# Optimization experiments

Measured on AMD Instinct MI355X. Metric: run time of the kernel, lower is better.

Reference implementation:

```python
import jax, jax.numpy as jnp
import numpy as np

VOCAB = 50000
DIM = 20      # vector_dim; must equal RNN hidden size per the classifier shape constraint
HID = 20
NCLS = 5
B, S = 16384, 256

def setup_inputs() -> dict:
    key = jax.random.key(0)
    k1, k2, k3, k4, k5, k6 = jax.random.split(key, 6)
    x = jax.random.randint(k1, (B, S), 0, VOCAB, dtype=jnp.int64)
    emb = jax.random.normal(k2, (VOCAB, DIM), dtype=jnp.float32)
    W_ih = jax.random.normal(k3, (HID, DIM), dtype=jnp.float32) * 0.1
    W_hh = jax.random.normal(k4, (HID, HID), dtype=jnp.float32) * 0.1
    W_cls = jax.random.normal(k5, (NCLS, DIM), dtype=jnp.float32) * 0.1
    b_cls = jax.random.normal(k6, (NCLS,), dtype=jnp.float32) * 0.1
    return {"x": x, "emb": emb, "W_ih": W_ih, "W_hh": W_hh, "W_cls": W_cls, "b_cls": b_cls}

def reference(x, emb, W_ih, W_hh, W_cls, b_cls):
    # padding_idx=0: row 0 of embedding is zero
    emb = emb.at[0].set(0.0)
    xe = emb[x]                                   # [B, S, DIM]
    # precompute input projection for all timesteps in one big matmul
    xp = jnp.einsum('bsd,hd->sbh', xe, W_ih)      # [S, B, HID]
    h0 = jnp.zeros((x.shape[0], HID), dtype=xe.dtype)

    def step(h, xt):
        h = jnp.tanh(xt + h @ W_hh.T)
        return h, None

    h_last, _ = jax.lax.scan(step, h0, xp)        # [B, HID]
    y_pred = h_last @ W_cls.T + b_cls             # [B, 5]
    return y_pred
```

## Files before the change

kernel.cpp:

```cpp
#include <hip/hip_runtime.h>
#include <hip/hip_bf16.h>

#define SEQ  256
#define DIM  20
#define NCLS 5
#define ALPHA 2.8853900817779268f

typedef short  bf16x8 __attribute__((ext_vector_type(8)));
typedef float  f32x4  __attribute__((ext_vector_type(4)));
typedef float  v2f    __attribute__((ext_vector_type(2)));

__device__ __forceinline__ v2f fast_tanh2_s(v2f xs) {
    v2f e;
    e.x = __builtin_amdgcn_exp2f(xs.x);
    e.y = __builtin_amdgcn_exp2f(xs.y);
    v2f d = e + 1.0f;
    const float r = __builtin_amdgcn_rcpf(d.x * d.y);
    v2f inv;
    inv.x = d.y * r;
    inv.y = d.x * r;
    return __builtin_elementwise_fma((v2f)(-2.0f), inv, (v2f)(1.0f));
}

__device__ __forceinline__ int cvt_pk_bf16(float lo, float hi) {
    int r;
    asm("v_cvt_pk_bf16_f32 %0, %1, %2" : "=v"(r) : "v"(lo), "v"(hi));
    return r;
}

__device__ __forceinline__ void pl32swap(int &a, int &b) {
    asm("v_permlane32_swap_b32 %0, %1" : "+v"(a), "+v"(b));
}

__device__ __forceinline__ int permk(int k) {
    return (k >= 4 && k < 8) ? k + 4 : (k >= 8 && k < 12) ? k - 4 : k;
}

union I4B { int i[4]; bf16x8 f; };

#define STEP(TIDX)                                                            \
    {                                                                          \
        const f32x4 loN = *(const f32x4*)(emb + (size_t)tokG0 * DIM + eoff0);  \
        const f32x4 hiN = *(const f32x4*)(emb + (size_t)tokG0 * DIM + eoff1);  \
        const bool  nzN = (tokG0 != 0);                                        \
        const int tokNew = xp[(TIDX)];                                         \
        const f32x4 acc1 = __builtin_amdgcn_mfma_f32_16x16x32_bf16(A1h, Bh.f, aePre1, 0, 0, 0); \
        const f32x4 acc0 = __builtin_amdgcn_mfma_f32_16x16x32_bf16(A0h, Bh.f, aePre0, 0, 0, 0); \
        I4B Be;                                                                \
        Be.i[0] = nzA ? cvt_pk_bf16(loA[0], loA[1]) : 0;                       \
        Be.i[1] = nzA ? cvt_pk_bf16(loA[2], loA[3]) : 0;                       \
        Be.i[2] = nzA ? cvt_pk_bf16(hiA[0], hiA[1]) : 0;                       \
        Be.i[3] = nzA ? cvt_pk_bf16(hiA[2], hiA[3]) : 0;                       \
        aePre0 = __builtin_amdgcn_mfma_f32_16x16x32_bf16(A0e, Be.f, zf, 0, 0, 0); \
        aePre1 = __builtin_amdgcn_mfma_f32_16x16x32_bf16(A1e, Be.f, zf, 0, 0, 0); \
        const v2f p2 = fast_tanh2_s((v2f){acc1[0], acc1[1]});                  \
        const v2f p3 = fast_tanh2_s((v2f){acc1[2], acc1[3]});                  \
        int tp0 = cvt_pk_bf16(p2.x, p2.y);                                     \
        int tp1 = cvt_pk_bf16(p3.x, p3.y);                                     \
        const v2f p0 = fast_tanh2_s((v2f){acc0[0], acc0[1]});                  \
        const v2f p1 = fast_tanh2_s((v2f){acc0[2], acc0[3]});                  \
        int w0 = cvt_pk_bf16(p0.x, p0.y);                                      \
        int w1 = cvt_pk_bf16(p1.x, p1.y);                                      \
        pl32swap(w0, tp0);                 \
        pl32swap(w1, tp1);                                                     \
        Bh.i[0] = w0; Bh.i[1] = w1; Bh.i[2] = tp0; Bh.i[3] = tp1;              \
        loA = loB; hiA = hiB; nzA = nzB;                                       \
        loB = loC; hiB = hiC; nzB = nzC;                                       \
        loC = loD; hiC = hiD; nzC = nzD;                                       \
        loD = loN; hiD = hiN; nzD = nzN;                                       \
        tokG0 = tokG1; tokG1 = tokG2; tokG2 = tokG3; tokG3 = tokNew;           \
    }

__global__ __launch_bounds__(256)
__attribute__((amdgpu_waves_per_eu(1, 1)))
void rnn_mfma(const int* __restrict__ x,
              const float* __restrict__ emb,
              const float* __restrict__ W_ih,
              const float* __restrict__ W_hh,
              const float* __restrict__ W_cls,
              const float* __restrict__ b_cls,
              float* __restrict__ out, int B)
{
    const int gtid = blockIdx.x * blockDim.x + threadIdx.x;
    const int wave = gtid >> 6;
    const int lane = (int)(threadIdx.x & 63);
    const int c = lane & 15;
    const int q = lane >> 4;
    const int row0 = wave * 16;
    if (row0 >= B) return;

    auto loadA = [&](const float* M, int U0, int ROWS, bool pk, float scale) {
        bf16x8 f;
        const int uu = U0 + c;
        const int ur = uu < ROWS ? uu : 0;
#pragma unroll
        for (int j = 0; j < 8; ++j) {
            const int kk = 8 * q + j;
            const int kp = pk ? permk(kk) : kk;
            const int kr = kp < DIM ? kp : 0;
            float v = M[ur * DIM + kr] * scale;
            v = (uu < ROWS && kk < DIM) ? v : 0.0f;
            __hip_bfloat16 hb = __float2bfloat16(v);
            f[j] = *reinterpret_cast<short*>(&hb);
        }
        return f;
    };
    const bf16x8 A0h = loadA(W_hh,  0, DIM,  true,  ALPHA);
    const bf16x8 A0e = loadA(W_ih,  0, DIM,  false, ALPHA);
    const bf16x8 A1h = loadA(W_hh, 16, DIM,  true,  ALPHA);
    const bf16x8 A1e = loadA(W_ih, 16, DIM,  false, ALPHA);
    const bf16x8 Acl = loadA(W_cls, 0, NCLS, true,  1.0f);

    float bias[4];
#pragma unroll
    for (int j = 0; j < 4; ++j) {
        const int idx = 4 * q + j;
        bias[j] = (idx < NCLS) ? b_cls[idx] : 0.0f;
    }

    const int eoff0 = (q == 0) ? 0 : (q == 1) ? 8 : 16;
    const int eoff1 = (q == 0) ? 4 : (q == 1) ? 12 : 16;

    const int* xp = x + (size_t)(row0 + c) * SEQ;
    const f32x4 zf = {0.0f, 0.0f, 0.0f, 0.0f};

    I4B Bh; Bh.i[0] = Bh.i[1] = Bh.i[2] = Bh.i[3] = 0;
    const int tk0 = xp[0];
    const int tk1 = xp[1];
    const int tk2 = xp[2];
    const int tk3 = xp[3];
    const int tk4 = xp[4];
    f32x4 aePre0, aePre1;
    {
        const f32x4 lo = *(const f32x4*)(emb + (size_t)tk0 * DIM + eoff0);
        const f32x4 hi = *(const f32x4*)(emb + (size_t)tk0 * DIM + eoff1);
        const bool nz = (tk0 != 0);
        I4B Be;
        Be.i[0] = nz ? cvt_pk_bf16(lo[0], lo[1]) : 0;
        Be.i[1] = nz ? cvt_pk_bf16(lo[2], lo[3]) : 0;
        Be.i[2] = nz ? cvt_pk_bf16(hi[0], hi[1]) : 0;
        Be.i[3] = nz ? cvt_pk_bf16(hi[2], hi[3]) : 0;
        aePre0 = __builtin_amdgcn_mfma_f32_16x16x32_bf16(A0e, Be.f, zf, 0, 0, 0);
        aePre1 = __builtin_amdgcn_mfma_f32_16x16x32_bf16(A1e, Be.f, zf, 0, 0, 0);
    }

    f32x4 loA, hiA, loB, hiB, loC, hiC, loD, hiD;
    bool nzA, nzB, nzC, nzD;
    loA = *(const f32x4*)(emb + (size_t)tk1 * DIM + eoff0);
    hiA = *(const f32x4*)(emb + (size_t)tk1 * DIM + eoff1);
    nzA = (tk1 != 0);
    loB = *(const f32x4*)(emb + (size_t)tk2 * DIM + eoff0);
    hiB = *(const f32x4*)(emb + (size_t)tk2 * DIM + eoff1);
    nzB = (tk2 != 0);
    loC = *(const f32x4*)(emb + (size_t)tk3 * DIM + eoff0);
    hiC = *(const f32x4*)(emb + (size_t)tk3 * DIM + eoff1);
    nzC = (tk3 != 0);
    loD = *(const f32x4*)(emb + (size_t)tk4 * DIM + eoff0);
    hiD = *(const f32x4*)(emb + (size_t)tk4 * DIM + eoff1);
    nzD = (tk4 != 0);
    int tokG0 = xp[5];
    int tokG1 = xp[6];
    int tokG2 = xp[7];
    int tokG3 = xp[8];

#pragma unroll 8
    for (int s = 0; s < 240; ++s) {
        STEP(s + 9)
    }
#pragma unroll 4
    for (int s = 240; s < SEQ; ++s) {
        STEP((s + 9 < SEQ) ? (s + 9) : (SEQ - 1))
    }

    const f32x4 y = __builtin_amdgcn_mfma_f32_16x16x32_bf16(Acl, Bh.f, zf, 0, 0, 0);
    float* orow = out + (size_t)(row0 + c) * NCLS;
    if (q == 0) {
        orow[0] = y[0] + bias[0];
        orow[1] = y[1] + bias[1];
        orow[2] = y[2] + bias[2];
        orow[3] = y[3] + bias[3];
    } else if (q == 1) {
        orow[4] = y[0] + bias[0];
    }
}

extern "C" void kernel_launch(void* const* d_in, const int* in_sizes, int n_in,
                              void* d_out, int out_size, void* d_ws, size_t ws_size,
                              hipStream_t stream) {
    const int*   x     = (const int*)d_in[0];
    const float* emb   = (const float*)d_in[1];
    const float* W_ih  = (const float*)d_in[2];
    const float* W_hh  = (const float*)d_in[3];
    const float* W_cls = (const float*)d_in[4];
    const float* b_cls = (const float*)d_in[5];
    float* out = (float*)d_out;

    const int B = in_sizes[0] / SEQ;
    const int threads = B * 4;
    const int block = 256;
    const int grid = (threads + block - 1) / block;
    rnn_mfma<<<grid, block, 0, stream>>>(x, emb, W_ih, W_hh, W_cls, b_cls, out, B);
}
```

Before: 68.56 us.

## Interleave two independent 16-row RNN tiles per wave to hide MFMA latency

Each wave now processes two independent 16-row batch tiles (P and Q) and interleaves their gather, MFMA, tanh and rotate phases so one tile's work fills the other's recurrence dependency stalls. The launch changes from 256-thread blocks with one tile per wave to 64-thread blocks with two tiles per wave, which halves the wave count. This costs roughly double the register state per wave, fewer resident waves overall, and assumes B is a multiple of 32.

```diff
diff --git a/kernel.cpp b/kernel.cpp
--- a/kernel.cpp
+++ b/kernel.cpp
@@ -38,56 +38,113 @@
 
 union I4B { int i[4]; bf16x8 f; };
 
-#define STEP(TIDX)                                                            \
-    {                                                                          \
-        const f32x4 loN = *(const f32x4*)(emb + (size_t)tokG0 * DIM + eoff0);  \
-        const f32x4 hiN = *(const f32x4*)(emb + (size_t)tokG0 * DIM + eoff1);  \
-        const bool  nzN = (tokG0 != 0);                                        \
-        const int tokNew = xp[(TIDX)];                                         \
-        const f32x4 acc1 = __builtin_amdgcn_mfma_f32_16x16x32_bf16(A1h, Bh.f, aePre1, 0, 0, 0); \
-        const f32x4 acc0 = __builtin_amdgcn_mfma_f32_16x16x32_bf16(A0h, Bh.f, aePre0, 0, 0, 0); \
+#define TILE_PROLOG(S, XP)                                                     \
+    I4B Bh##S; Bh##S.i[0] = Bh##S.i[1] = Bh##S.i[2] = Bh##S.i[3] = 0;          \
+    f32x4 aePre0##S, aePre1##S;                                                \
+    {                                                                          \
+        const int tk0 = (XP)[0];                                               \
+        const f32x4 lo = *(const f32x4*)(emb + (size_t)tk0 * DIM + eoff0);     \
+        const f32x4 hi = *(const f32x4*)(emb + (size_t)tk0 * DIM + eoff1);     \
+        const bool nz = (tk0 != 0);                       \
         I4B Be;                                                                \
-        Be.i[0] = nzA ? cvt_pk_bf16(loA[0], loA[1]) : 0;                       \
-        Be.i[1] = nzA ? cvt_pk_bf16(loA[2], loA[3]) : 0;                       \
-        Be.i[2] = nzA ? cvt_pk_bf16(hiA[0], hiA[1]) : 0;                       \
-        Be.i[3] = nzA ? cvt_pk_bf16(hiA[2], hiA[3]) : 0;                       \
-        aePre0 = __builtin_amdgcn_mfma_f32_16x16x32_bf16(A0e, Be.f, zf, 0, 0, 0); \
-        aePre1 = __builtin_amdgcn_mfma_f32_16x16x32_bf16(A1e, Be.f, zf, 0, 0, 0); \
-        const v2f p2 = fast_tanh2_s((v2f){acc1[0], acc1[1]});                  \
-        const v2f p3 = fast_tanh2_s((v2f){acc1[2], acc1[3]});                  \
+        Be.i[0] = nz ? cvt_pk_bf16(lo[0], lo[1]) : 0;                          \
+        Be.i[1] = nz ? cvt_pk_bf16(lo[2], lo[3]) : 0;                          \
+        Be.i[2] = nz ? cvt_pk_bf16(hi[0], hi[1]) : 0;                          \
+        Be.i[3] = nz ? cvt_pk_bf16(hi[2], hi[3]) : 0;                          \
+        aePre0##S = __builtin_amdgcn_mfma_f32_16x16x32_bf16(A0e, Be.f, zf, 0, 0, 0); \
+        aePre1##S = __builtin_amdgcn_mfma_f32_16x16x32_bf16(A1e, Be.f, zf, 0, 0, 0); \
+    }                                                                          \
+    const int tk1##S = (XP)[1], tk2##S = (XP)[2], tk3##S = (XP)[3], tk4##S = (XP)[4]; \
+    f32x4 loA##S, hiA##S, loB##S, hiB##S, loC##S, hiC##S, loD##S, hiD##S;      \
+    bool nzA##S, nzB##S, nzC##S, nzD##S;                                       \
+    loA##S = *(const f32x4*)(emb + (size_t)tk1##S * DIM + eoff0);              \
+    hiA##S = *(const f32x4*)(emb + (size_t)tk1##S * DIM + eoff1);              \
+    nzA##S = (tk1##S != 0);                                                    \
+    loB##S = *(const f32x4*)(emb + (size_t)tk2##S * DIM + eoff0);              \
+    hiB##S = *(const f32x4*)(emb + (size_t)tk2##S * DIM + eoff1);              \
+    nzB##S = (tk2##S != 0);                                                    \
+    loC##S = *(const f32x4*)(emb + (size_t)tk3##S * DIM + eoff0);              \
+    hiC##S = *(const f32x4*)(emb + (size_t)tk3##S * DIM + eoff1);              \
+    nzC##S = (tk3##S != 0);                                                    \
+    loD##S = *(const f32x4*)(emb + (size_t)tk4##S * DIM + eoff0);              \
+    hiD##S = *(const f32x4*)(emb + (size_t)tk4##S * DIM + eoff1);              \
+    nzD##S = (tk4##S != 0);                                                    \
+    int tokG0##S = (XP)[5], tokG1##S = (XP)[6], tokG2##S = (XP)[7], tokG3##S = (XP)[8];
+
+#define PH_GATHER(S, TIDX)                                                     \
+    const f32x4 loN##S = *(const f32x4*)(emb + (size_t)tokG0##S * DIM + eoff0);\
+    const f32x4 hiN##S = *(const f32x4*)(emb + (size_t)tokG0##S * DIM + eoff1);\
+    const bool  nzN##S = (tokG0##S != 0);                                      \
+    const int tokNew##S = xp##S[(TIDX)];
+
+#define PH_HMFMA(S)                                                            \
+    const f32x4 acc1##S = __builtin_amdgcn_mfma_f32_16x16x32_bf16(A1h, Bh##S.f, aePre1##S, 0, 0, 0); \
+    const f32x4 acc0##S = __builtin_amdgcn_mfma_f32_16x16x32_bf16(A0h, Bh##S.f, aePre0##S, 0, 0, 0);
+
+#define PH_EPATH(S)                                                            \
+    {                                                                          \
+        I4B Be;                                                                \
+        Be.i[0] = nzA##S ? cvt_pk_bf16(loA##S[0], loA##S[1]) : 0;              \
+        Be.i[1] = nzA##S ? cvt_pk_bf16(loA##S[2], loA##S[3]) : 0;              \
+        Be.i[2] = nzA##S ? cvt_pk_bf16(hiA##S[0], hiA##S[1]) : 0;              \
+        Be.i[3] = nzA##S ? cvt_pk_bf16(hiA##S[2], hiA##S[3]) : 0;              \
+        aePre0##S = __builtin_amdgcn_mfma_f32_16x16x32_bf16(A0e, Be.f, zf, 0, 0, 0); \
+        aePre1##S = __builtin_amdgcn_mfma_f32_16x16x32_bf16(A1e, Be.f, zf, 0, 0, 0); \
+    }
+
+#define PH_TANH(S)                                                             \
+    {                                                                          \
+        const v2f p2 = fast_tanh2_s((v2f){acc1##S[0], acc1##S[1]});            \
+        const v2f p3 = fast_tanh2_s((v2f){acc1##S[2], acc1##S[3]});            \
         int tp0 = cvt_pk_bf16(p2.x, p2.y);                                     \
         int tp1 = cvt_pk_bf16(p3.x, p3.y);                                     \
-        const v2f p0 = fast_tanh2_s((v2f){acc0[0], acc0[1]});                  \
-        const v2f p1 = fast_tanh2_s((v2f){acc0[2], acc0[3]});                  \
+        const v2f p0 = fast_tanh2_s((v2f){acc0##S[0], acc0##S[1]});            \
+        const v2f p1 = fast_tanh2_s((v2f){acc0##S[2], acc0##S[3]});            \
         int w0 = cvt_pk_bf16(p0.x, p0.y);                                      \
         int w1 = cvt_pk_bf16(p1.x, p1.y);                                      \
         pl32swap(w0, tp0);                 \
         pl32swap(w1, tp1);                                                     \
-        Bh.i[0] = w0; Bh.i[1] = w1; Bh.i[2] = tp0; Bh.i[3] = tp1;              \
-        loA = loB; hiA = hiB; nzA = nzB;                                       \
-        loB = loC; hiB = hiC; nzB = nzC;                                       \
-        loC = loD; hiC = hiD; nzC = nzD;                                       \
-        loD = loN; hiD = hiN; nzD = nzN;                                       \
-        tokG0 = tokG1; tokG1 = tokG2; tokG2 = tokG3; tokG3 = tokNew;           \
-    }
-
-__global__ __launch_bounds__(256)
+        Bh##S.i[0] = w0; Bh##S.i[1] = w1; Bh##S.i[2] = tp0; Bh##S.i[3] = tp1;  \
+    }
+
+#define PH_ROT(S)                                                              \
+    loA##S = loB##S; hiA##S = hiB##S; nzA##S = nzB##S;                         \
+    loB##S = loC##S; hiB##S = hiC##S; nzB##S = nzC##S;                         \
+    loC##S = loD##S; hiC##S = hiD##S; nzC##S = nzD##S;                         \
+    loD##S = loN##S; hiD##S = hiN##S; nzD##S = nzN##S;                         \
+    tokG0##S = tokG1##S; tokG1##S = tokG2##S; tokG2##S = tokG3##S; tokG3##S = tokNew##S;
+
+#define STEP2(TIDX)                                                            \
+    {                                                                          \
+        PH_GATHER(P, TIDX)                                                     \
+        PH_GATHER(Q, TIDX)                                                     \
+        PH_HMFMA(P)                                                            \
+        PH_HMFMA(Q)                                                            \
+        PH_EPATH(P)                                                            \
+        PH_EPATH(Q)                                                            \
+        PH_TANH(P)                                                             \
+        PH_TANH(Q)                                                             \
+        PH_ROT(P)                                                              \
+        PH_ROT(Q)                                                              \
+    }
+
+__global__ __launch_bounds__(64)
 __attribute__((amdgpu_waves_per_eu(1, 1)))
-void rnn_mfma(const int* __restrict__ x,
-              const float* __restrict__ emb,
-              const float* __restrict__ W_ih,
-              const float* __restrict__ W_hh,
-              const float* __restrict__ W_cls,
-              const float* __restrict__ b_cls,
-              float* __restrict__ out, int B)
+void rnn_mfma2(const int* __restrict__ x,
+               const float* __restrict__ emb,
+               const float* __restrict__ W_ih,
+               const float* __restrict__ W_hh,
+               const float* __restrict__ W_cls,
+               const float* __restrict__ b_cls,
+               float* __restrict__ out, int B)
 {
-    const int gtid = blockIdx.x * blockDim.x + threadIdx.x;
-    const int wave = gtid >> 6;
+    const int wave = (int)blockIdx.x;
     const int lane = (int)(threadIdx.x & 63);
     const int c = lane & 15;
     const int q = lane >> 4;
-    const int row0 = wave * 16;
-    if (row0 >= B) return;
+    const int row0P = wave * 32;
+    const int row0Q = row0P + 16;
+    if (row0P >= B) return;
 
     auto loadA = [&](const float* M, int U0, int ROWS, bool pk, float scale) {
         bf16x8 f;
@@ -121,66 +178,45 @@
     const int eoff0 = (q == 0) ? 0 : (q == 1) ? 8 : 16;
     const int eoff1 = (q == 0) ? 4 : (q == 1) ? 12 : 16;
 
-    const int* xp = x + (size_t)(row0 + c) * SEQ;
+    const int* xpP = x + (size_t)(row0P + c) * SEQ;
+    const int* xpQ = x + (size_t)(row0Q + c) * SEQ;
     const f32x4 zf = {0.0f, 0.0f, 0.0f, 0.0f};
 
-    I4B Bh; Bh.i[0] = Bh.i[1] = Bh.i[2] = Bh.i[3] = 0;
-    const int tk0 = xp[0];
-    const int tk1 = xp[1];
-    const int tk2 = xp[2];
-    const int tk3 = xp[3];
-    const int tk4 = xp[4];
-    f32x4 aePre0, aePre1;
-    {
-        const f32x4 lo = *(const f32x4*)(emb + (size_t)tk0 * DIM + eoff0);
-        const f32x4 hi = *(const f32x4*)(emb + (size_t)tk0 * DIM + eoff1);
-        const bool nz = (tk0 != 0);
-        I4B Be;
-        Be.i[0] = nz ? cvt_pk_bf16(lo[0], lo[1]) : 0;
-        Be.i[1] = nz ? cvt_pk_bf16(lo[2], lo[3]) : 0;
-        Be.i[2] = nz ? cvt_pk_bf16(hi[0], hi[1]) : 0;
-        Be.i[3] = nz ? cvt_pk_bf16(hi[2], hi[3]) : 0;
-        aePre0 = __builtin_amdgcn_mfma_f32_16x16x32_bf16(A0e, Be.f, zf, 0, 0, 0);
-        aePre1 = __builtin_amdgcn_mfma_f32_16x16x32_bf16(A1e, Be.f, zf, 0, 0, 0);
-    }
-
-    f32x4 loA, hiA, loB, hiB, loC, hiC, loD, hiD;
-    bool nzA, nzB, nzC, nzD;
-    loA = *(const f32x4*)(emb + (size_t)tk1 * DIM + eoff0);
-    hiA = *(const f32x4*)(emb + (size_t)tk1 * DIM + eoff1);
-    nzA = (tk1 != 0);
-    loB = *(const f32x4*)(emb + (size_t)tk2 * DIM + eoff0);
-    hiB = *(const f32x4*)(emb + (size_t)tk2 * DIM + eoff1);
-    nzB = (tk2 != 0);
-    loC = *(const f32x4*)(emb + (size_t)tk3 * DIM + eoff0);
-    hiC = *(const f32x4*)(emb + (size_t)tk3 * DIM + eoff1);
-    nzC = (tk3 != 0);
-    loD = *(const f32x4*)(emb + (size_t)tk4 * DIM + eoff0);
-    hiD = *(const f32x4*)(emb + (size_t)tk4 * DIM + eoff1);
-    nzD = (tk4 != 0);
-    int tokG0 = xp[5];
-    int tokG1 = xp[6];
-    int tokG2 = xp[7];
-    int tokG3 = xp[8];
-
-#pragma unroll 8
+    TILE_PROLOG(P, xpP)
+    TILE_PROLOG(Q, xpQ)
+
+#pragma unroll 4
     for (int s = 0; s < 240; ++s) {
-        STEP(s + 9)
+        STEP2(s + 9)
     }
 #pragma unroll 4
     for (int s = 240; s < SEQ; ++s) {
-        STEP((s + 9 < SEQ) ? (s + 9) : (SEQ - 1))
-    }
-
-    const f32x4 y = __builtin_amdgcn_mfma_f32_16x16x32_bf16(Acl, Bh.f, zf, 0, 0, 0);
-    float* orow = out + (size_t)(row0 + c) * NCLS;
-    if (q == 0) {
-        orow[0] = y[0] + bias[0];
-        orow[1] = y[1] + bias[1];
-        orow[2] = y[2] + bias[2];
-        orow[3] = y[3] + bias[3];
-    } else if (q == 1) {
-        orow[4] = y[0] + bias[0];
+        STEP2((s + 9 < SEQ) ? (s + 9) : (SEQ - 1))
+    }
+
+    const f32x4 yP = __builtin_amdgcn_mfma_f32_16x16x32_bf16(Acl, BhP.f, zf, 0, 0, 0);
+    const f32x4 yQ = __builtin_amdgcn_mfma_f32_16x16x32_bf16(Acl, BhQ.f, zf, 0, 0, 0);
+    {
+        float* orow = out + (size_t)(row0P + c) * NCLS;
+        if (q == 0) {
+            orow[0] = yP[0] + bias[0];
+            orow[1] = yP[1] + bias[1];
+            orow[2] = yP[2] + bias[2];
+            orow[3] = yP[3] + bias[3];
+        } else if (q == 1) {
+            orow[4] = yP[0] + bias[0];
+        }
+    }
+    {
+        float* orow = out + (size_t)(row0Q + c) * NCLS;
+        if (q == 0) {
+            orow[0] = yQ[0] + bias[0];
+            orow[1] = yQ[1] + bias[1];
+            orow[2] = yQ[2] + bias[2];
+            orow[3] = yQ[3] + bias[3];
+        } else if (q == 1) {
+            orow[4] = yQ[0] + bias[0];
+        }
     }
 }
 
@@ -196,8 +232,6 @@
     float* out = (float*)d_out;
 
     const int B = in_sizes[0] / SEQ;
-    const int threads = B * 4;
-    const int block = 256;
-    const int grid = (threads + block - 1) / block;
-    rnn_mfma<<<grid, block, 0, stream>>>(x, emb, W_ih, W_hh, W_cls, b_cls, out, B);
-}
+    const int waves = (B + 31) / 32;
+    rnn_mfma2<<<waves, 64, 0, stream>>>(x, emb, W_ih, W_hh, W_cls, b_cls, out, B);
+}
```

New measurement: 117.9 us. 1.72x slower.
